# Kernel tuning notes

Measured on AMD Instinct MI355X. Metric: run time of the kernel, lower is better.

The kernel has to match this reference:

```python
import jax, jax.numpy as jnp
import numpy as np

N_NODES = 100000
N_EDGES = 1000000
IN_DIM, HID_DIM, OUT_DIM = 256, 128, 128


def setup_inputs() -> dict:
    key = jax.random.key(0)
    ks = jax.random.split(key, 6)
    return {
        "x1": jax.random.normal(ks[0], (N_NODES, IN_DIM), jnp.float32),
        "edge_index1": jax.random.randint(ks[1], (2, N_EDGES), 0, N_NODES, jnp.int64),
        "x2": jax.random.normal(ks[2], (N_NODES, IN_DIM), jnp.float32),
        "edge_index2": jax.random.randint(ks[3], (2, N_EDGES), 0, N_NODES, jnp.int64),
        "W0": jax.random.normal(ks[4], (IN_DIM, HID_DIM), jnp.float32) * (1.0 / np.sqrt(IN_DIM)),
        "b0": jnp.zeros((HID_DIM,), jnp.float32),
        "W1": jax.random.normal(ks[5], (HID_DIM, OUT_DIM), jnp.float32) * (1.0 / np.sqrt(HID_DIM)),
        "b1": jnp.zeros((OUT_DIM,), jnp.float32),
        "p1": 0,
        "p2": 0,
    }


def _gcn_backbone(x, edge_index, W0, b0, W1, b1):
    # PyG GCNConv: add self-loops, symmetric norm D^-1/2 (A+I) D^-1/2,
    # h = x @ W, aggregate src->dst, add bias.
    n = x.shape[0]
    loops = jnp.arange(n, dtype=edge_index.dtype)
    src = jnp.concatenate([edge_index[0], loops])
    dst = jnp.concatenate([edge_index[1], loops])
    deg = jax.ops.segment_sum(jnp.ones_like(dst, jnp.float32), dst, num_segments=n)
    dinv = jnp.where(deg > 0, jax.lax.rsqrt(deg), 0.0)
    coef = (dinv[src] * dinv[dst])[:, None]  # [E+n, 1]

    def conv(h, W, b):
        h = h @ W  # [n, d_out]
        return jax.ops.segment_sum(h[src] * coef, dst, num_segments=n) + b

    h = jax.nn.relu(conv(x, W0, b0))
    # dropout with p=0 / eval mode is identity
    return conv(h, W1, b1)


def _colnorm(h):
    # (h - mean(0)) / std(0), torch std is unbiased (ddof=1)
    mu = h.mean(axis=0)
    sd = h.std(axis=0, ddof=1)
    return (h - mu) / sd


def reference(x1, edge_index1, x2, edge_index2, W0, b0, W1, b1, p1, p2):
    h1 = _gcn_backbone(x1, edge_index1, W0, b0, W1, b1)
    h2 = _gcn_backbone(x2, edge_index2, W0, b0, W1, b1)
    return _colnorm(h1), _colnorm(h2)
```

## Files before the change

kernel.cpp:

```cpp
#include <hip/hip_runtime.h>

#define CDIV(a,b) (((a)+(b)-1)/(b))

typedef __bf16 bf16x8 __attribute__((ext_vector_type(8)));
typedef float  f32x4  __attribute__((ext_vector_type(4)));

__device__ __forceinline__ ushort f2bf(float f) {
    uint u = __float_as_uint(f);
    uint r = u + 0x7fffu + ((u >> 16) & 1u);
    return (ushort)(r >> 16);
}
__device__ __forceinline__ float bf_lo(uint p) { return __uint_as_float(p << 16); }
__device__ __forceinline__ float bf_hi(uint p) { return __uint_as_float(p & 0xffff0000u); }


__global__ __launch_bounds__(256) void binA_k(const int* __restrict__ src,
                                              const int* __restrict__ dst, int E,
                                              int NB, int CAP,
                                              int* __restrict__ bcur,
                                              uint* __restrict__ binned) {
    __shared__ uint hist[512];
    __shared__ uint cur[512];
    const int t = threadIdx.x;
    for (int i = t; i < NB; i += 256) hist[i] = 0;
    __syncthreads();

    const int e0 = blockIdx.x * 4096;
    const int e1 = min(e0 + 4096, E);
    for (int e = e0 + t; e < e1; e += 256)
        atomicAdd(&hist[dst[e] >> 8], 1u);
    __syncthreads();

    for (int i = t; i < NB; i += 256) {
        uint c = hist[i];
        cur[i] = c ? (uint)atomicAdd(&bcur[i], (int)c) : 0u;
    }
    __syncthreads();

    for (int e = e0 + t; e < e1; e += 256) {
        int d = dst[e];
        int b = d >> 8;
        uint p = atomicAdd(&cur[b], 1u);
        if (p < (uint)CAP)
            binned[(size_t)b * CAP + p] = ((uint)src[e] << 8) | (uint)(d & 255);
    }
}

__global__ __launch_bounds__(256) void binB_k(const uint* __restrict__ binned,
                                              const int* __restrict__ bcur,
                                              int N, int CAP,
                                              int* __restrict__ csr,
                                              int* __restrict__ start,
                                              int* __restrict__ degc,
                                              float* __restrict__ dinv) {
    __shared__ uint hist[256];
    __shared__ uint cur[256];
    __shared__ uint wsum[4];
    const int b = blockIdx.x;
    const int t = threadIdx.x;
    int cnt = bcur[b];
    if (cnt > CAP) cnt = CAP;
    const uint* be = binned + (size_t)b * CAP;

    hist[t] = 0;
    __syncthreads();
    for (int e = t; e < cnt; e += 256) atomicAdd(&hist[be[e] & 255u], 1u);
    __syncthreads();

    uint v = hist[t];
    uint inc = v;
#pragma unroll
    for (int off = 1; off < 64; off <<= 1) {
        uint n = __shfl_up(inc, off);
        if ((t & 63) >= off) inc += n;
    }
    if ((t & 63) == 63) wsum[t >> 6] = inc;
    __syncthreads();
    uint wo = 0;
    if ((t >> 6) >= 1) wo += wsum[0];
    if ((t >> 6) >= 2) wo += wsum[1];
    if ((t >> 6) >= 3) wo += wsum[2];
    uint excl = wo + inc - v;
    cur[t] = excl;
    __syncthreads();

    const int base = b * CAP;
    for (int e = t; e < cnt; e += 256) {
        uint w = be[e];
        uint p = atomicAdd(&cur[w & 255u], 1u);
        csr[base + (int)p] = (int)(w >> 8);
    }

    int node = b * 256 + t;
    if (node < N) {
        start[node] = base + (int)excl;
        degc[node]  = (int)v;
        dinv[node]  = rsqrtf((float)(v + 1));
    }
}


__global__ __launch_bounds__(256) void pack_w_k(const float* __restrict__ W,
                                                ushort* __restrict__ Wp, int K) {
    int idx = blockIdx.x * 256 + threadIdx.x;
    int total = (K / 32) * 8 * 64;
    if (idx >= total) return;
    int l  = idx & 63;
    int nf = (idx >> 6) & 7;
    int kb = idx >> 9;
    int col = nf * 16 + (l & 15);
    int k0  = kb * 32 + (l >> 4) * 8;
    ushort o[8];
#pragma unroll
    for (int j = 0; j < 8; ++j) o[j] = f2bf(W[(size_t)(k0 + j) * 128 + col]);
    *reinterpret_cast<float4*>(Wp + (size_t)idx * 8) = *reinterpret_cast<float4*>(o);
}


template <int K, typename TIn>
__global__ __launch_bounds__(256) void gemm_mfma(const TIn* __restrict__ X,
                                                 const float4* __restrict__ Wp,
                                                 const float* __restrict__ dinv,
                                                 ushort* __restrict__ C, int N) {
    const int lane = threadIdx.x & 63;
    const int w    = threadIdx.x >> 6;
    const int r0   = blockIdx.x * 128 + w * 32;

    const int arow0 = r0 + (lane & 15);
    const int kc    = lane >> 4;

    f32x4 acc[2][8] = {};

#pragma unroll
    for (int kb = 0; kb < K / 32; ++kb) {
        bf16x8 bfr[8];
#pragma unroll
        for (int nf = 0; nf < 8; ++nf)
            bfr[nf] = *reinterpret_cast<const bf16x8*>(Wp + (size_t)(kb * 8 + nf) * 64 + lane);

        bf16x8 afr[2];
#pragma unroll
        for (int mf = 0; mf < 2; ++mf) {
            int row = arow0 + mf * 16;
            bf16x8 a = {};
            if (row < N) {
                if constexpr (sizeof(TIn) == 4) {
                    const float* pa = (const float*)X + (size_t)row * K + kb * 32 + kc * 8;
                    float4 v0 = *reinterpret_cast<const float4*>(pa);
                    float4 v1 = *reinterpret_cast<const float4*>(pa + 4);
                    a[0] = (__bf16)v0.x; a[1] = (__bf16)v0.y;
                    a[2] = (__bf16)v0.z; a[3] = (__bf16)v0.w;
                    a[4] = (__bf16)v1.x; a[5] = (__bf16)v1.y;
                    a[6] = (__bf16)v1.z; a[7] = (__bf16)v1.w;
                } else {
                    const ushort* pa = (const ushort*)X + (size_t)row * K + kb * 32 + kc * 8;
                    a = *reinterpret_cast<const bf16x8*>(pa);
                }
            }
            afr[mf] = a;
        }

#pragma unroll
        for (int mf = 0; mf < 2; ++mf)
#pragma unroll
            for (int nf = 0; nf < 8; ++nf)
                acc[mf][nf] = __builtin_amdgcn_mfma_f32_16x16x32_bf16(afr[mf], bfr[nf], acc[mf][nf], 0, 0, 0);
    }

#pragma unroll
    for (int mf = 0; mf < 2; ++mf) {
        const int rb = r0 + mf * 16 + ((lane >> 4) << 2);
#pragma unroll
        for (int i = 0; i < 4; ++i) {
            int row = rb + i;
            if (row < N) {
                float dr = dinv[row];
#pragma unroll
                for (int nf = 0; nf < 8; ++nf)
                    C[(size_t)row * 128 + nf * 16 + (lane & 15)] = f2bf(acc[mf][nf][i] * dr);
            }
        }
    }
}


template <int RELU, typename TOut>
__global__ __launch_bounds__(256) void agg_k(const ushort* __restrict__ Hin,
                                             TOut* __restrict__ Hout,
                                             const int* __restrict__ csr,
                                             const int* __restrict__ start,
                                             const int* __restrict__ degc,
                                             const float* __restrict__ dinv,
                                             const float* __restrict__ bias,
                                             int N) {
    const int wid  = threadIdx.x >> 6;
    const int lane = threadIdx.x & 63;
    const int v = blockIdx.x * 4 + wid;
    if (v >= N) return;

    float dv = dinv[v];
    int s   = start[v];
    int end = s + degc[v];

    const uint* base = reinterpret_cast<const uint*>(Hin);
    uint hp = base[(size_t)v * 64 + lane];
    float ax = bf_lo(hp);
    float ay = bf_hi(hp);

    for (int bs = s; bs < end; bs += 64) {
        int m = end - bs;
        if (m > 64) m = 64;
        int u_l = 0;
        if (lane < m) u_l = csr[bs + lane];
        int e = 0;
        for (; e + 8 <= m; e += 8) {
            uint p[8];
#pragma unroll
            for (int j = 0; j < 8; ++j) {
                int u = __shfl(u_l, e + j);
                p[j] = base[(size_t)u * 64 + lane];
            }
#pragma unroll
            for (int j = 0; j < 8; ++j) { ax += bf_lo(p[j]); ay += bf_hi(p[j]); }
        }
        if (e + 4 <= m) {
            uint p[4];
#pragma unroll
            for (int j = 0; j < 4; ++j) {
                int u = __shfl(u_l, e + j);
                p[j] = base[(size_t)u * 64 + lane];
            }
#pragma unroll
            for (int j = 0; j < 4; ++j) { ax += bf_lo(p[j]); ay += bf_hi(p[j]); }
            e += 4;
        }
        for (; e < m; ++e) {
            int u = __shfl(u_l, e);
            uint p = base[(size_t)u * 64 + lane];
            ax += bf_lo(p);
            ay += bf_hi(p);
        }
    }

    float2 b = reinterpret_cast<const float2*>(bias)[lane];
    float ox = fmaf(dv, ax, b.x);
    float oy = fmaf(dv, ay, b.y);
    if (RELU) {
        ox = fmaxf(ox, 0.f);
        oy = fmaxf(oy, 0.f);
    }
    if constexpr (sizeof(TOut) == 2) {
        uint packed = (uint)f2bf(ox) | ((uint)f2bf(oy) << 16);
        reinterpret_cast<uint*>(Hout)[(size_t)v * 64 + lane] = packed;
    } else {
        reinterpret_cast<float2*>(Hout)[(size_t)v * 64 + lane] = make_float2(ox, oy);
    }
}


__global__ __launch_bounds__(256) void colstats_k(const ushort* __restrict__ H,
                                                  float* __restrict__ stats, int N) {
    __shared__ float4 red[4][64];
    const int t  = threadIdx.x;
    const int cp = t & 63;
    const int rg = t >> 6;
    const int r0 = blockIdx.x * 512;
    const int r1 = min(r0 + 512, N);

    const uint* base = reinterpret_cast<const uint*>(H);
    float sx = 0.f, qx = 0.f, sy = 0.f, qy = 0.f;
    for (int r = r0 + rg; r < r1; r += 4) {
        uint p = base[(size_t)r * 64 + cp];
        float a = bf_lo(p), b = bf_hi(p);
        sx += a; qx = fmaf(a, a, qx);
        sy += b; qy = fmaf(b, b, qy);
    }
    red[rg][cp] = make_float4(sx, qx, sy, qy);
    __syncthreads();
    if (rg == 0) {
        float4 a0 = red[0][cp], a1 = red[1][cp], a2 = red[2][cp], a3 = red[3][cp];
        float* st = stats + (size_t)(blockIdx.x & 7) * 256;
        atomicAdd(&st[cp * 2],           a0.x + a1.x + a2.x + a3.x);
        atomicAdd(&st[cp * 2 + 1],       a0.z + a1.z + a2.z + a3.z);
        atomicAdd(&st[128 + cp * 2],     a0.y + a1.y + a2.y + a3.y);
        atomicAdd(&st[128 + cp * 2 + 1], a0.w + a1.w + a2.w + a3.w);
    }
}


__global__ __launch_bounds__(256) void colnorm_k(const ushort* __restrict__ H,
                                                 const float* __restrict__ stats,
                                                 float* __restrict__ Out, int N) {
    __shared__ float mu_s[128], rs_s[128];
    const int t = threadIdx.x;
    if (t < 128) {
        float s = 0.f, q = 0.f;
#pragma unroll
        for (int sl = 0; sl < 8; ++sl) {
            s += stats[sl * 256 + t];
            q += stats[sl * 256 + 128 + t];
        }
        float mu = s / (float)N;
        float var = (q - s * mu) / (float)(N - 1);
        mu_s[t] = mu;
        rs_s[t] = rsqrtf(var);
    }
    __syncthreads();

    size_t total = (size_t)N * 16;
    size_t stride = (size_t)gridDim.x * 256;
    for (size_t i = (size_t)blockIdx.x * 256 + t; i < total; i += stride) {
        uint4 p = reinterpret_cast<const uint4*>(H)[i];
        int c0 = ((int)(i & 15)) * 8;
        float o[8] = {bf_lo(p.x), bf_hi(p.x), bf_lo(p.y), bf_hi(p.y),
                      bf_lo(p.z), bf_hi(p.z), bf_lo(p.w), bf_hi(p.w)};
        float4 r0, r1;
        r0.x = (o[0] - mu_s[c0 + 0]) * rs_s[c0 + 0];
        r0.y = (o[1] - mu_s[c0 + 1]) * rs_s[c0 + 1];
        r0.z = (o[2] - mu_s[c0 + 2]) * rs_s[c0 + 2];
        r0.w = (o[3] - mu_s[c0 + 3]) * rs_s[c0 + 3];
        r1.x = (o[4] - mu_s[c0 + 4]) * rs_s[c0 + 4];
        r1.y = (o[5] - mu_s[c0 + 5]) * rs_s[c0 + 5];
        r1.z = (o[6] - mu_s[c0 + 6]) * rs_s[c0 + 6];
        r1.w = (o[7] - mu_s[c0 + 7]) * rs_s[c0 + 7];
        reinterpret_cast<float4*>(Out)[i * 2]     = r0;
        reinterpret_cast<float4*>(Out)[i * 2 + 1] = r1;
    }
}


extern "C" void kernel_launch(void* const* d_in, const int* in_sizes, int n_in,
                              void* d_out, int out_size, void* d_ws, size_t ws_size,
                              hipStream_t stream) {
    const float* x1  = (const float*)d_in[0];
    const int*   ei1 = (const int*)d_in[1];
    const float* x2  = (const float*)d_in[2];
    const int*   ei2 = (const int*)d_in[3];
    const float* W0  = (const float*)d_in[4];
    const float* b0  = (const float*)d_in[5];
    const float* W1  = (const float*)d_in[6];
    const float* b1  = (const float*)d_in[7];

    const int N  = in_sizes[0] / 256;
    const int E1 = in_sizes[1] / 2;
    const int E2 = in_sizes[3] / 2;
    const int Emax = E1 > E2 ? E1 : E2;

    const int NB  = CDIV(N, 256);
    int cap = (Emax / NB) * 8 / 5 + 1024;
    const int CAP = (cap + 1023) & ~1023;

    char* base = (char*)d_ws;
    size_t off = 0;
    auto carve = [&](size_t bytes) -> char* {
        char* p = base + off;
        off = (off + bytes + 255) & ~(size_t)255;
        return p;
    };
    ushort* hA    = (ushort*)carve((size_t)N * 128 * 2);
    ushort* hB    = (ushort*)carve((size_t)N * 128 * 2);
    float*  dinv  = (float*)carve((size_t)N * 4);
    int*    degc  = (int*)carve((size_t)N * 4);
    int*    startA= (int*)carve((size_t)N * 4);
    int*    csr   = (int*)carve((size_t)NB * CAP * 4);
    ushort* Wp0   = (ushort*)carve((256 / 32) * 8 * 64 * 8 * 2);
    ushort* Wp1   = (ushort*)carve((128 / 32) * 8 * 64 * 8 * 2);
    float*  stats = (float*)carve(8 * 256 * 4);
    int*    bcur  = (int*)carve((size_t)NB * 4);
    uint*   binned = (uint*)hA;

    pack_w_k<<<CDIV((256 / 32) * 8 * 64, 256), 256, 0, stream>>>(W0, Wp0, 256);
    pack_w_k<<<CDIV((128 / 32) * 8 * 64, 256), 256, 0, stream>>>(W1, Wp1, 128);

    for (int g = 0; g < 2; ++g) {
        const float* x  = g ? x2 : x1;
        const int*   ei = g ? ei2 : ei1;
        const int    E  = g ? E2 : E1;
        float* outg = (float*)d_out + (size_t)g * N * 128;

        hipMemsetAsync(bcur, 0, (size_t)NB * 4, stream);
        hipMemsetAsync(stats, 0, 8 * 256 * 4, stream);

        binA_k<<<CDIV(E, 4096), 256, 0, stream>>>(ei, ei + E, E, NB, CAP, bcur, binned);
        binB_k<<<NB, 256, 0, stream>>>(binned, bcur, N, CAP, csr, startA, degc, dinv);

        gemm_mfma<256, float><<<CDIV(N, 128), 256, 0, stream>>>(
            x, (const float4*)Wp0, dinv, hA, N);
        agg_k<1, ushort><<<CDIV(N, 4), 256, 0, stream>>>(
            hA, hB, csr, startA, degc, dinv, b0, N);

        gemm_mfma<128, ushort><<<CDIV(N, 128), 256, 0, stream>>>(
            hB, (const float4*)Wp1, dinv, hA, N);
        agg_k<0, ushort><<<CDIV(N, 4), 256, 0, stream>>>(
            hA, hB, csr, startA, degc, dinv, b1, N);

        colstats_k<<<CDIV(N, 512), 256, 0, stream>>>(hB, stats, N);
        colnorm_k<<<1024, 256, 0, stream>>>(hB, stats, outg, N);
    }
}
```

Before: 502.6 us.

## Stage GEMM A tiles through swizzled LDS with register prefetch double buffering

The GEMM now loads each A row chunk with fully coalesced global reads (4 threads per 32-element row slice), converts it to bf16 and writes it into an XOR-swizzled, double-buffered shared-memory tile. The next k-block is prefetched into registers while the current one feeds the MFMAs. The block tile shrinks from 128 to 64 rows, with one 16-row MFMA fragment per wave, which doubles the grid. This targets the strided per-lane global A loads and latency stalls of the old direct-to-register path, at the cost of a barrier per k-step and halved W-fragment reuse per wave.

```diff
diff --git a/kernel.cpp b/kernel.cpp
--- a/kernel.cpp
+++ b/kernel.cpp
@@ -122,63 +122,83 @@
                                                  const float4* __restrict__ Wp,
                                                  const float* __restrict__ dinv,
                                                  ushort* __restrict__ C, int N) {
-    const int lane = threadIdx.x & 63;
-    const int w    = threadIdx.x >> 6;
-    const int r0   = blockIdx.x * 128 + w * 32;
-
-    const int arow0 = r0 + (lane & 15);
-    const int kc    = lane >> 4;
-
-    f32x4 acc[2][8] = {};
-
-#pragma unroll
-    for (int kb = 0; kb < K / 32; ++kb) {
-        bf16x8 bfr[8];
-#pragma unroll
-        for (int nf = 0; nf < 8; ++nf)
-            bfr[nf] = *reinterpret_cast<const bf16x8*>(Wp + (size_t)(kb * 8 + nf) * 64 + lane);
-
-        bf16x8 afr[2];
-#pragma unroll
-        for (int mf = 0; mf < 2; ++mf) {
-            int row = arow0 + mf * 16;
-            bf16x8 a = {};
-            if (row < N) {
-                if constexpr (sizeof(TIn) == 4) {
-                    const float* pa = (const float*)X + (size_t)row * K + kb * 32 + kc * 8;
-                    float4 v0 = *reinterpret_cast<const float4*>(pa);
-                    float4 v1 = *reinterpret_cast<const float4*>(pa + 4);
-                    a[0] = (__bf16)v0.x; a[1] = (__bf16)v0.y;
-                    a[2] = (__bf16)v0.z; a[3] = (__bf16)v0.w;
-                    a[4] = (__bf16)v1.x; a[5] = (__bf16)v1.y;
-                    a[6] = (__bf16)v1.z; a[7] = (__bf16)v1.w;
-                } else {
-                    const ushort* pa = (const ushort*)X + (size_t)row * K + kb * 32 + kc * 8;
-                    a = *reinterpret_cast<const bf16x8*>(pa);
-                }
+    constexpr int KB = K / 32;
+    __shared__ ushort As[2][64 * 32];
+
+    const int t    = threadIdx.x;
+    const int lane = t & 63;
+    const int w    = t >> 6;
+    const int row0 = blockIdx.x * 64;
+
+    const int sr    = t >> 2;
+    const int sk    = t & 3;
+    const int sslot = sk ^ ((sr >> 1) & 3);
+    const size_t sgoff = (size_t)min(row0 + sr, N - 1) * K + sk * 8;
+    ushort* sdst = &As[0][sr * 32 + sslot * 8];
+
+    const int mr    = w * 16 + (lane & 15);
+    const int mkc   = lane >> 4;
+    const int mslot = mkc ^ ((mr >> 1) & 3);
+    const ushort* msrc = &As[0][mr * 32 + mslot * 8];
+
+    f32x4 acc[8] = {};
+
+    float4 v0, v1;
+    uint4  ub;
+
+#define LOADX(kb_)                                                              \
+    do {                                                                        \
+        if constexpr (sizeof(TIn) == 4) {                                       \
+            const float* p = (const float*)X + sgoff + (kb_) * 32;              \
+            v0 = *reinterpret_cast<const float4*>(p);                           \
+            v1 = *reinterpret_cast<const float4*>(p + 4);                       \
+        } else {                                                                \
+            const ushort* p = (const ushort*)X + sgoff + (kb_) * 32;            \
+            ub = *reinterpret_cast<const uint4*>(p);                            \
+        }                                                                       \
+    } while (0)
+
+    LOADX(0);
+#pragma unroll
+    for (int kb = 0; kb < KB; ++kb) {
+        const int buf = kb & 1;
+        {
+            ushort av[8];
+            if constexpr (sizeof(TIn) == 4) {
+                av[0] = f2bf(v0.x); av[1] = f2bf(v0.y);
+                av[2] = f2bf(v0.z); av[3] = f2bf(v0.w);
+                av[4] = f2bf(v1.x); av[5] = f2bf(v1.y);
+                av[6] = f2bf(v1.z); av[7] = f2bf(v1.w);
+            } else {
+                *reinterpret_cast<uint4*>(av) = ub;
             }
-            afr[mf] = a;
-        }
-
-#pragma unroll
-        for (int mf = 0; mf < 2; ++mf)
+            *reinterpret_cast<float4*>(sdst + buf * (64 * 32)) =
+                *reinterpret_cast<float4*>(av);
+        }
+        if (kb + 1 < KB) LOADX(kb + 1);
+
+        asm volatile("s_waitcnt lgkmcnt(0)" ::: "memory");
+        __builtin_amdgcn_s_barrier();
+        __builtin_amdgcn_sched_barrier(0);
+
+        bf16x8 a = *reinterpret_cast<const bf16x8*>(msrc + buf * (64 * 32));
+#pragma unroll
+        for (int nf = 0; nf < 8; ++nf) {
+            bf16x8 b = *reinterpret_cast<const bf16x8*>(Wp + (size_t)(kb * 8 + nf) * 64 + lane);
+            acc[nf] = __builtin_amdgcn_mfma_f32_16x16x32_bf16(a, b, acc[nf], 0, 0, 0);
+        }
+    }
+#undef LOADX
+
+    const int rb = row0 + w * 16 + ((lane >> 4) << 2);
+#pragma unroll
+    for (int i = 0; i < 4; ++i) {
+        int row = rb + i;
+        if (row < N) {
+            float dr = dinv[row];
 #pragma unroll
             for (int nf = 0; nf < 8; ++nf)
-                acc[mf][nf] = __builtin_amdgcn_mfma_f32_16x16x32_bf16(afr[mf], bfr[nf], acc[mf][nf], 0, 0, 0);
-    }
-
-#pragma unroll
-    for (int mf = 0; mf < 2; ++mf) {
-        const int rb = r0 + mf * 16 + ((lane >> 4) << 2);
-#pragma unroll
-        for (int i = 0; i < 4; ++i) {
-            int row = rb + i;
-            if (row < N) {
-                float dr = dinv[row];
-#pragma unroll
-                for (int nf = 0; nf < 8; ++nf)
-                    C[(size_t)row * 128 + nf * 16 + (lane & 15)] = f2bf(acc[mf][nf][i] * dr);
-            }
+                C[(size_t)row * 128 + nf * 16 + (lane & 15)] = f2bf(acc[nf][i] * dr);
         }
     }
 }
@@ -384,12 +404,12 @@
         binA_k<<<CDIV(E, 4096), 256, 0, stream>>>(ei, ei + E, E, NB, CAP, bcur, binned);
         binB_k<<<NB, 256, 0, stream>>>(binned, bcur, N, CAP, csr, startA, degc, dinv);
 
-        gemm_mfma<256, float><<<CDIV(N, 128), 256, 0, stream>>>(
+        gemm_mfma<256, float><<<CDIV(N, 64), 256, 0, stream>>>(
             x, (const float4*)Wp0, dinv, hA, N);
         agg_k<1, ushort><<<CDIV(N, 4), 256, 0, stream>>>(
             hA, hB, csr, startA, degc, dinv, b0, N);
 
-        gemm_mfma<128, ushort><<<CDIV(N, 128), 256, 0, stream>>>(
+        gemm_mfma<128, ushort><<<CDIV(N, 64), 256, 0, stream>>>(
             hB, (const float4*)Wp1, dinv, hA, N);
         agg_k<0, ushort><<<CDIV(N, 4), 256, 0, stream>>>(
             hA, hB, csr, startA, degc, dinv, b1, N);
```

New measurement: 499.9 us. Within noise of the previous version (-0.5%).
